# Optimization experiments

Hardware: AMD Instinct MI355X
Metric: run time of the kernel (lower is better)

## Reference

```python
import jax, jax.numpy as jnp
import numpy as np

CAPACITY_RATIO = 0.75  # matches init kwarg


def setup_inputs() -> dict:
    key = jax.random.key(0)
    k1, k2, k3 = jax.random.split(key, 3)
    B, L, D = 4, 8192, 1024
    x = jax.random.normal(k1, (B, L, D), dtype=jnp.float32)
    # router: nn.Linear(dim, 1, bias=False) -> weight vector [D]
    w_router = jax.random.normal(k2, (D,), dtype=jnp.float32) * 0.02
    # block_fn instantiated as GELU(Linear(D, D)) applied to selected tokens
    w_block = jax.random.normal(k3, (D, D), dtype=jnp.float32) * 0.02
    return {"x": x, "w_router": w_router, "w_block": w_block}


def reference(x, w_router, w_block):
    # Inference path of MoDRouter.forward (self.training == False)
    B, L, D = x.shape
    k = max(1, int(L * CAPACITY_RATIO))  # 6144 < L, so routing path taken
    # scores = self.router(x).squeeze(-1)  -> [B, L]
    scores = jnp.einsum('bld,d->bl', x, w_router)
    # top-k token selection per batch row
    _, top_idx = jax.lax.top_k(scores, k)  # [B, k]
    # gather selected tokens: [B, k, D]
    selected = jnp.take_along_axis(x, top_idx[:, :, None], axis=1)
    # block_fn(selected, None): GELU(selected @ w_block)
    processed = jax.nn.gelu(jnp.einsum('bkd,de->bke', selected, w_block))
    # scatter processed tokens back; unselected tokens pass through (residual skip)
    batch_idx = jnp.arange(B)[:, None]  # [B, 1]
    out = x.at[batch_idx, top_idx].set(processed)
    return out
```

## Files before the change

### kernel.cpp

```cpp
#include <hip/hip_runtime.h>
#include <hip/hip_bf16.h>

typedef unsigned short u16;
typedef unsigned int u32;
typedef __attribute__((ext_vector_type(8))) short short8;
typedef __attribute__((ext_vector_type(4))) float f32x4;

#define L_TOK 8192
#define BATCH 4
#define DIM 1024
#define KSEL 6144
#define NTOK (BATCH * L_TOK)
#define NSEL (BATCH * KSEL)
#define NUNSEL (NTOK - NSEL)

__device__ __forceinline__ u16 f2bf(float f) {
    u32 u = __float_as_uint(f);
    return (u16)((u + 0x7fffu + ((u >> 16) & 1u)) >> 16);
}
__device__ __forceinline__ u32 cvt2(float a, float b) {
    __hip_bfloat162 h = __float22bfloat162_rn(float2{a, b});
    u32 r;
    __builtin_memcpy(&r, &h, 4);
    return r;
}
__device__ __forceinline__ float gelu_fast(float v) {
    float z2 = 1.5957691216057308f * (v + 0.044715f * v * v * v);
    return v / (1.0f + __expf(-z2));
}
__device__ __forceinline__ void async_copy16(const void* g, void* l) {
    __builtin_amdgcn_global_load_lds(
        (const __attribute__((address_space(1))) void*)g,
        (__attribute__((address_space(3))) void*)l, 16, 0, 0);
}

__global__ __launch_bounds__(256) void score_kernel(const float* __restrict__ x,
                                                    const float* __restrict__ wr,
                                                    float* __restrict__ scores,
                                                    u16* __restrict__ xb) {
    int token = blockIdx.x * 4 + (threadIdx.x >> 6);
    int lane = threadIdx.x & 63;
    const float4* xr = (const float4*)(x + (size_t)token * DIM) + lane * 4;
    const float4* wp = (const float4*)wr + lane * 4;
    float4 v[4];
    double acc = 0.0;
#pragma unroll
    for (int c = 0; c < 4; ++c) {
        v[c] = xr[c];
        float4 wv = wp[c];
        acc += (double)v[c].x * wv.x + (double)v[c].y * wv.y +
               (double)v[c].z * wv.z + (double)v[c].w * wv.w;
    }
    if (xb) {
        union { short8 s[2]; u32 u[8]; } pk;
        pk.u[0] = cvt2(v[0].x, v[0].y); pk.u[1] = cvt2(v[0].z, v[0].w);
        pk.u[2] = cvt2(v[1].x, v[1].y); pk.u[3] = cvt2(v[1].z, v[1].w);
        pk.u[4] = cvt2(v[2].x, v[2].y); pk.u[5] = cvt2(v[2].z, v[2].w);
        pk.u[6] = cvt2(v[3].x, v[3].y); pk.u[7] = cvt2(v[3].z, v[3].w);
        short8* dst = (short8*)(xb + (size_t)token * DIM + lane * 16);
        dst[0] = pk.s[0]; dst[1] = pk.s[1];
    }
#pragma unroll
    for (int off = 32; off > 0; off >>= 1) acc += __shfl_down(acc, off, 64);
    if (lane == 0) scores[token] = (float)acc;
}

__global__ __launch_bounds__(1024) void select_kernel(const float* __restrict__ scores,
                                                      int* __restrict__ mask,
                                                      int* __restrict__ sel_idx,
                                                      int* __restrict__ unsel_idx) {
    __shared__ u32 keys[L_TOK];
    __shared__ int hist[256];
    __shared__ int g0[256], g1[256];
    __shared__ int wsum[16];
    __shared__ int wsum2[16];
    __shared__ int sel_digit, greater_cnt;
    const int b = blockIdx.x;
    const int tid = threadIdx.x;
    const int lane = tid & 63, wid = tid >> 6;
    const float* s = scores + (size_t)b * L_TOK;
    for (int i = tid; i < L_TOK; i += 1024) {
        u32 u = __float_as_uint(s[i]);
        keys[i] = (u & 0x80000000u) ? ~u : (u | 0x80000000u);
    }

    u32 prefix = 0;
    int need = KSEL;
#pragma unroll
    for (int pass = 0; pass < 4; ++pass) {
        const int shift = 24 - 8 * pass;
        const u32 pmask = (pass == 0) ? 0u : (0xFFFFFFFFu << (shift + 8));
        if (tid < 256) hist[tid] = 0;
        __syncthreads();
        for (int i = tid; i < L_TOK; i += 1024) {
            u32 key = keys[i];
            if ((key & pmask) == prefix)
                atomicAdd(&hist[(key >> shift) & 0xffu], 1);
        }
        __syncthreads();
        if (tid < 256) g0[tid] = hist[tid];
        __syncthreads();
        int* src = g0;
        int* dst = g1;
        for (int step = 1; step < 256; step <<= 1) {
            if (tid < 256) {
                int v = src[tid];
                if (tid + step < 256) v += src[tid + step];
                dst[tid] = v;
            }
            __syncthreads();
            int* t = src; src = dst; dst = t;
        }
        if (tid < 256) {
            int Gd = src[tid];
            int Gn = (tid == 255) ? 0 : src[tid + 1];
            if (Gd >= need && Gn < need) { sel_digit = tid; greater_cnt = Gn; }
        }
        __syncthreads();
        prefix |= ((u32)sel_digit) << shift;
        need -= greater_cnt;
        __syncthreads();
    }
    const u32 T = prefix;
    const int need_eq = need;

    const int base = tid * 8;
    u32 kv[8];
    int eq = 0;
#pragma unroll
    for (int c = 0; c < 8; ++c) { kv[c] = keys[base + c]; eq += (kv[c] == T); }
    int inc = eq;
#pragma unroll
    for (int off = 1; off < 64; off <<= 1) {
        int n = __shfl_up(inc, off, 64);
        if (lane >= off) inc += n;
    }
    if (lane == 63) wsum[wid] = inc;
    __syncthreads();
    int wbase = 0;
    for (int w = 0; w < wid; ++w) wbase += wsum[w];
    int rank = wbase + inc - eq;
    int sel[8];
#pragma unroll
    for (int c = 0; c < 8; ++c) {
        u32 key = kv[c];
        int se = 0;
        if (key > T) se = 1;
        else if (key == T) { se = (rank < need_eq) ? 1 : 0; rank++; }
        sel[c] = se;
    }
    int4* mp = (int4*)(mask + (size_t)b * L_TOK + base);
    mp[0] = int4{sel[0], sel[1], sel[2], sel[3]};
    mp[1] = int4{sel[4], sel[5], sel[6], sel[7]};

    int cnt = 0;
#pragma unroll
    for (int c = 0; c < 8; ++c) cnt += sel[c];
    int inc2 = cnt;
#pragma unroll
    for (int off = 1; off < 64; off <<= 1) {
        int n = __shfl_up(inc2, off, 64);
        if (lane >= off) inc2 += n;
    }
    if (lane == 63) wsum2[wid] = inc2;
    __syncthreads();
    int wb2 = 0;
    for (int w = 0; w < wid; ++w) wb2 += wsum2[w];
    int pos = wb2 + inc2 - cnt;
    int up = base - pos;
    int* si = sel_idx + (size_t)b * KSEL;
    int* ui = unsel_idx + (size_t)b * (L_TOK - KSEL);
#pragma unroll
    for (int c = 0; c < 8; ++c) {
        int gtok = b * L_TOK + base + c;
        if (sel[c]) si[pos++] = gtok;
        else        ui[up++]  = gtok;
    }
}

__global__ __launch_bounds__(256) void transpose_kernel(const float* __restrict__ W,
                                                        u16* __restrict__ WT) {
    __shared__ u16 tile[32][33];
    int bx = blockIdx.x * 32, by = blockIdx.y * 32;
    int tx = threadIdx.x & 31, ty = threadIdx.x >> 5;
    for (int r = ty; r < 32; r += 8)
        tile[r][tx] = f2bf(W[(size_t)(by + r) * DIM + bx + tx]);
    __syncthreads();
    for (int r = ty; r < 32; r += 8)
        WT[(size_t)(bx + r) * DIM + by + tx] = tile[tx][r];
}

#define PM 256
#define PN 128
#define PK 32
#define PNT (DIM / PK)
#define ASZ (PM * PK)
#define BSZ (PN * PK)

__global__ __launch_bounds__(256, 2) void gemm_idx_kernel(const u16* __restrict__ Xb,
                                                          const u16* __restrict__ WT,
                                                          const int* __restrict__ sel_idx,
                                                          float* __restrict__ out) {
    __shared__ alignas(16) u16 As[2][ASZ];
    __shared__ alignas(16) u16 Bs[2][BSZ];
    const int tid = threadIdx.x;
    const int wave = tid >> 6, lane = tid & 63;
    const int wm = wave >> 1, wn = wave & 1;
    const int rowbase = blockIdx.x * PM;
    const int colbase = blockIdx.y * PN;
    const int q = lane >> 4, mrow = lane & 15;

    f32x4 acc[8][4] = {};

    const u16* aS[4]; int aO[4];
    const u16* bS[2]; int bO[2];
#pragma unroll
    for (int j = 0; j < 4; ++j) {
        int c = tid + 256 * j;
        int row = c >> 2, slot = c & 3;
        int ss = slot ^ ((row >> 1) & 3);
        int tok = sel_idx[rowbase + row];
        aS[j] = Xb + (size_t)tok * DIM + ss * 8;
        aO[j] = c * 8;
    }
#pragma unroll
    for (int j = 0; j < 2; ++j) {
        int c = tid + 256 * j;
        int row = c >> 2, slot = c & 3;
        int ss = slot ^ ((row >> 1) & 3);
        bS[j] = WT + (size_t)(colbase + row) * DIM + ss * 8;
        bO[j] = c * 8;
    }

#pragma unroll
    for (int tt = 0; tt < 2; ++tt) {
        int ko = tt * PK;
#pragma unroll
        for (int j = 0; j < 4; ++j) async_copy16(aS[j] + ko, &As[tt][aO[j]]);
#pragma unroll
        for (int j = 0; j < 2; ++j) async_copy16(bS[j] + ko, &Bs[tt][bO[j]]);
    }
    asm volatile("s_waitcnt vmcnt(6)" ::: "memory");
    __builtin_amdgcn_sched_barrier(0);
    __builtin_amdgcn_s_barrier();
    __builtin_amdgcn_sched_barrier(0);

    const int xorv = (q ^ ((mrow >> 1) & 3)) * 8;

    for (int t = 0; t < PNT; ++t) {
        const u16* Ac = As[t & 1];
        const u16* Bc = Bs[t & 1];
        short8 a[8], b[4];
#pragma unroll
        for (int i = 0; i < 8; ++i) {
            int r = wm * 128 + i * 16 + mrow;
            a[i] = *(const short8*)(Ac + r * PK + xorv);
        }
#pragma unroll
        for (int j = 0; j < 4; ++j) {
            int r = wn * 64 + j * 16 + mrow;
            b[j] = *(const short8*)(Bc + r * PK + xorv);
        }
        asm volatile("s_waitcnt lgkmcnt(0)" ::: "memory");
        __builtin_amdgcn_sched_barrier(0);
        __builtin_amdgcn_s_barrier();
        __builtin_amdgcn_sched_barrier(0);

        {
            int ts = (t + 2 < PNT) ? t + 2 : t;
            int ko = ts * PK;
            u16* Aw = As[t & 1];
            u16* Bw = Bs[t & 1];
#pragma unroll
            for (int j = 0; j < 4; ++j) async_copy16(aS[j] + ko, Aw + aO[j]);
#pragma unroll
            for (int j = 0; j < 2; ++j) async_copy16(bS[j] + ko, Bw + bO[j]);
        }
        __builtin_amdgcn_sched_barrier(0);

        __builtin_amdgcn_s_setprio(1);
#pragma unroll
        for (int i = 0; i < 8; ++i)
#pragma unroll
            for (int j = 0; j < 4; ++j)
                acc[i][j] = __builtin_amdgcn_mfma_f32_16x16x32_bf16(a[i], b[j], acc[i][j], 0, 0, 0);
        __builtin_amdgcn_s_setprio(0);
        __builtin_amdgcn_sched_barrier(0);

        asm volatile("s_waitcnt vmcnt(6)" ::: "memory");
        __builtin_amdgcn_sched_barrier(0);
        __builtin_amdgcn_s_barrier();
        __builtin_amdgcn_sched_barrier(0);
    }

#pragma unroll
    for (int i = 0; i < 8; ++i) {
#pragma unroll
        for (int rr = 0; rr < 4; ++rr) {
            int lrow = wm * 128 + i * 16 + q * 4 + rr;
            int tok = sel_idx[rowbase + lrow];
#pragma unroll
            for (int j = 0; j < 4; ++j) {
                float g = gelu_fast(acc[i][j][rr]);
                int col = colbase + wn * 64 + j * 16 + mrow;
                out[(size_t)tok * DIM + col] = g;
            }
        }
    }
}

#define FBM 128
#define FBN 128
#define FBK 32
__global__ __launch_bounds__(256) void gemm_f32_kernel(const float* __restrict__ X,
                                                       const u16* __restrict__ WT,
                                                       const int* __restrict__ mask,
                                                       float* __restrict__ out) {
    __shared__ alignas(16) u16 Asf[FBM * FBK];
    __shared__ alignas(16) u16 Bsf[FBN * FBK];
    const int tid = threadIdx.x;
    const int wave = tid >> 6, lane = tid & 63;
    const int wm = wave >> 1, wn = wave & 1;
    const size_t rowbase = (size_t)blockIdx.x * FBM;
    const int colbase = blockIdx.y * FBN;

    f32x4 acc[4][4] = {};

    const int cb0 = tid, cb1 = tid + 256;
    const int br0 = cb0 >> 2, bk0 = (cb0 & 3) * 8;
    const int br1 = cb1 >> 2, bk1 = (cb1 & 3) * 8;
    const int arow = tid >> 1, ahalf = tid & 1;
    const int q = lane >> 4, mrow = lane & 15;

    for (int kt = 0; kt < DIM; kt += FBK) {
        async_copy16(WT + (size_t)(colbase + br0) * DIM + kt + bk0, Bsf + cb0 * 8);
        async_copy16(WT + (size_t)(colbase + br1) * DIM + kt + bk1, Bsf + cb1 * 8);

        const float4* xp = (const float4*)(X + (rowbase + arow) * DIM + kt + ahalf * 16);
        float4 v0 = xp[0], v1 = xp[1], v2 = xp[2], v3 = xp[3];
        union { short8 s[2]; u32 u[8]; } pk;
        pk.u[0] = cvt2(v0.x, v0.y); pk.u[1] = cvt2(v0.z, v0.w);
        pk.u[2] = cvt2(v1.x, v1.y); pk.u[3] = cvt2(v1.z, v1.w);
        pk.u[4] = cvt2(v2.x, v2.y); pk.u[5] = cvt2(v2.z, v2.w);
        pk.u[6] = cvt2(v3.x, v3.y); pk.u[7] = cvt2(v3.z, v3.w);
        *(short8*)(Asf + arow * FBK + ahalf * 16)     = pk.s[0];
        *(short8*)(Asf + arow * FBK + ahalf * 16 + 8) = pk.s[1];

        __syncthreads();

        short8 a[4], b[4];
#pragma unroll
        for (int i = 0; i < 4; ++i)
            a[i] = *(const short8*)(Asf + (wm * 64 + i * 16 + mrow) * FBK + q * 8);
#pragma unroll
        for (int j = 0; j < 4; ++j)
            b[j] = *(const short8*)(Bsf + (wn * 64 + j * 16 + mrow) * FBK + q * 8);
#pragma unroll
        for (int i = 0; i < 4; ++i)
#pragma unroll
            for (int j = 0; j < 4; ++j)
                acc[i][j] = __builtin_amdgcn_mfma_f32_16x16x32_bf16(a[i], b[j], acc[i][j], 0, 0, 0);
        __syncthreads();
    }

#pragma unroll
    for (int i = 0; i < 4; ++i) {
#pragma unroll
        for (int r = 0; r < 4; ++r) {
            size_t grow = rowbase + wm * 64 + i * 16 + q * 4 + r;
            if (mask[grow]) {
#pragma unroll
                for (int j = 0; j < 4; ++j) {
                    float g = gelu_fast(acc[i][j][r]);
                    int col = colbase + wn * 64 + j * 16 + mrow;
                    out[grow * DIM + col] = g;
                }
            }
        }
    }
}

__global__ __launch_bounds__(256) void passthrough_idx_kernel(const float* __restrict__ x,
                                                              const int* __restrict__ unsel_idx,
                                                              float* __restrict__ out) {
    int tok = unsel_idx[blockIdx.x];
    size_t c = (size_t)tok * (DIM / 4) + threadIdx.x;
    ((float4*)out)[c] = ((const float4*)x)[c];
}

extern "C" void kernel_launch(void* const* d_in, const int* in_sizes, int n_in,
                              void* d_out, int out_size, void* d_ws, size_t ws_size,
                              hipStream_t stream) {
    const float* x  = (const float*)d_in[0];
    const float* wr = (const float*)d_in[1];
    const float* wb = (const float*)d_in[2];
    float* out = (float*)d_out;

    char* ws = (char*)d_ws;
    float* scores    = (float*)ws;
    int*   mask      = (int*)(ws + (size_t)NTOK * 4);
    int*   sel_idx   = (int*)(ws + (size_t)NTOK * 8);
    int*   unsel_idx = (int*)(ws + (size_t)NTOK * 8 + (size_t)NSEL * 4);
    char*  after_idx = ws + (size_t)NTOK * 8 + (size_t)NTOK * 4;
    u16*   WT        = (u16*)after_idx;
    u16*   Xb        = (u16*)(after_idx + (size_t)DIM * DIM * 2);

    const size_t need_ws = (size_t)NTOK * 12 + (size_t)DIM * DIM * 2
                         + (size_t)NTOK * DIM * 2;
    const bool big = (ws_size >= need_ws);

    score_kernel<<<NTOK / 4, 256, 0, stream>>>(x, wr, scores, big ? Xb : nullptr);
    select_kernel<<<BATCH, 1024, 0, stream>>>(scores, mask, sel_idx, unsel_idx);
    transpose_kernel<<<dim3(DIM / 32, DIM / 32), 256, 0, stream>>>(wb, WT);
    if (big) {
        gemm_idx_kernel<<<dim3(NSEL / PM, DIM / PN), 256, 0, stream>>>(Xb, WT, sel_idx, out);
    } else {
        gemm_f32_kernel<<<dim3(NTOK / FBM, DIM / FBN), 256, 0, stream>>>(x, WT, mask, out);
    }
    passthrough_idx_kernel<<<NUNSEL, 256, 0, stream>>>(x, unsel_idx, out);
}
```

Baseline: 329.0 us.

## Replace double-buffered PK=32 GEMM pipeline with single-buffer PK=64 loop

Drops the two-stage async-copy double buffer and its manual waitcnt/barrier scheduling in the gathered GEMM. Instead it loads a 64-wide K tile into a single LDS buffer with a wider XOR swizzle, then runs two MFMA sub-steps per tile separated by __syncthreads. This halves the number of outer iterations and barriers and simplifies scheduling. In exchange, global loads no longer overlap with MFMA compute within a block, so the kernel relies on the second resident block to hide latency.

```diff
diff --git a/kernel.cpp b/kernel.cpp
--- a/kernel.cpp
+++ b/kernel.cpp
@@ -192,17 +192,14 @@
 
 #define PM 256
 #define PN 128
-#define PK 32
-#define PNT (DIM / PK)
-#define ASZ (PM * PK)
-#define BSZ (PN * PK)
+#define PK 64
 
 __global__ __launch_bounds__(256, 2) void gemm_idx_kernel(const u16* __restrict__ Xb,
                                                           const u16* __restrict__ WT,
                                                           const int* __restrict__ sel_idx,
                                                           float* __restrict__ out) {
-    __shared__ alignas(16) u16 As[2][ASZ];
-    __shared__ alignas(16) u16 Bs[2][BSZ];
+    __shared__ alignas(16) u16 As[PM * PK];
+    __shared__ alignas(16) u16 Bs[PN * PK];
     const int tid = threadIdx.x;
     const int wave = tid >> 6, lane = tid & 63;
     const int wm = wave >> 1, wn = wave & 1;
@@ -212,85 +209,54 @@
 
     f32x4 acc[8][4] = {};
 
-    const u16* aS[4]; int aO[4];
-    const u16* bS[2]; int bO[2];
-#pragma unroll
-    for (int j = 0; j < 4; ++j) {
+    const u16* aS[8]; int aO[8];
+    const u16* bS[4]; int bO[4];
+#pragma unroll
+    for (int j = 0; j < 8; ++j) {
         int c = tid + 256 * j;
-        int row = c >> 2, slot = c & 3;
-        int ss = slot ^ ((row >> 1) & 3);
+        int row = c >> 3, slot = c & 7;
+        int ss = slot ^ (row & 7);
         int tok = sel_idx[rowbase + row];
         aS[j] = Xb + (size_t)tok * DIM + ss * 8;
         aO[j] = c * 8;
     }
 #pragma unroll
-    for (int j = 0; j < 2; ++j) {
+    for (int j = 0; j < 4; ++j) {
         int c = tid + 256 * j;
-        int row = c >> 2, slot = c & 3;
-        int ss = slot ^ ((row >> 1) & 3);
+        int row = c >> 3, slot = c & 7;
+        int ss = slot ^ (row & 7);
         bS[j] = WT + (size_t)(colbase + row) * DIM + ss * 8;
         bO[j] = c * 8;
     }
 
-#pragma unroll
-    for (int tt = 0; tt < 2; ++tt) {
-        int ko = tt * PK;
-#pragma unroll
-        for (int j = 0; j < 4; ++j) async_copy16(aS[j] + ko, &As[tt][aO[j]]);
-#pragma unroll
-        for (int j = 0; j < 2; ++j) async_copy16(bS[j] + ko, &Bs[tt][bO[j]]);
-    }
-    asm volatile("s_waitcnt vmcnt(6)" ::: "memory");
-    __builtin_amdgcn_sched_barrier(0);
-    __builtin_amdgcn_s_barrier();
-    __builtin_amdgcn_sched_barrier(0);
-
-    const int xorv = (q ^ ((mrow >> 1) & 3)) * 8;
-
-    for (int t = 0; t < PNT; ++t) {
-        const u16* Ac = As[t & 1];
-        const u16* Bc = Bs[t & 1];
-        short8 a[8], b[4];
-#pragma unroll
-        for (int i = 0; i < 8; ++i) {
-            int r = wm * 128 + i * 16 + mrow;
-            a[i] = *(const short8*)(Ac + r * PK + xorv);
-        }
-#pragma unroll
-        for (int j = 0; j < 4; ++j) {
-            int r = wn * 64 + j * 16 + mrow;
-            b[j] = *(const short8*)(Bc + r * PK + xorv);
-        }
-        asm volatile("s_waitcnt lgkmcnt(0)" ::: "memory");
-        __builtin_amdgcn_sched_barrier(0);
-        __builtin_amdgcn_s_barrier();
-        __builtin_amdgcn_sched_barrier(0);
-
-        {
-            int ts = (t + 2 < PNT) ? t + 2 : t;
-            int ko = ts * PK;
-            u16* Aw = As[t & 1];
-            u16* Bw = Bs[t & 1];
-#pragma unroll
-            for (int j = 0; j < 4; ++j) async_copy16(aS[j] + ko, Aw + aO[j]);
-#pragma unroll
-            for (int j = 0; j < 2; ++j) async_copy16(bS[j] + ko, Bw + bO[j]);
-        }
-        __builtin_amdgcn_sched_barrier(0);
-
-        __builtin_amdgcn_s_setprio(1);
-#pragma unroll
-        for (int i = 0; i < 8; ++i)
-#pragma unroll
-            for (int j = 0; j < 4; ++j)
-                acc[i][j] = __builtin_amdgcn_mfma_f32_16x16x32_bf16(a[i], b[j], acc[i][j], 0, 0, 0);
-        __builtin_amdgcn_s_setprio(0);
-        __builtin_amdgcn_sched_barrier(0);
-
-        asm volatile("s_waitcnt vmcnt(6)" ::: "memory");
-        __builtin_amdgcn_sched_barrier(0);
-        __builtin_amdgcn_s_barrier();
-        __builtin_amdgcn_sched_barrier(0);
+    for (int kt = 0; kt < DIM; kt += PK) {
+#pragma unroll
+        for (int j = 0; j < 8; ++j) async_copy16(aS[j] + kt, As + aO[j]);
+#pragma unroll
+        for (int j = 0; j < 4; ++j) async_copy16(bS[j] + kt, Bs + bO[j]);
+        __syncthreads();
+
+#pragma unroll
+        for (int kk = 0; kk < 2; ++kk) {
+            const int xs = ((kk * 4 + q) ^ (mrow & 7)) * 8;
+            short8 a[8], b[4];
+#pragma unroll
+            for (int i = 0; i < 8; ++i) {
+                int r = wm * 128 + i * 16 + mrow;
+                a[i] = *(const short8*)(As + r * PK + xs);
+            }
+#pragma unroll
+            for (int j = 0; j < 4; ++j) {
+                int r = wn * 64 + j * 16 + mrow;
+                b[j] = *(const short8*)(Bs + r * PK + xs);
+            }
+#pragma unroll
+            for (int i = 0; i < 8; ++i)
+#pragma unroll
+                for (int j = 0; j < 4; ++j)
+                    acc[i][j] = __builtin_amdgcn_mfma_f32_16x16x32_bf16(a[i], b[j], acc[i][j], 0, 0, 0);
+        }
+        __syncthreads();
     }
 
 #pragma unroll
```

Result: no change. 325.8 us (-1.0%).
